# Performance work log

Hardware: AMD Instinct MI355X
Metric: run time of the kernel (lower is better)

The kernel has to match this reference:

```python
import jax, jax.numpy as jnp
import numpy as np

B, N_FED, INPUT_DIM, LATENT_DIM = 8192, 16384, 1024, 512


def setup_inputs() -> dict:
    key = jax.random.key(0)
    k1, k2, k3 = jax.random.split(key, 3)
    enc = jax.random.normal(k1, (B, LATENT_DIM), dtype=jnp.float32)
    X_fed = jax.random.normal(k2, (N_FED, INPUT_DIM), dtype=jnp.float32)
    # torch.rand -> uniform [0, 1)
    domain_diff = jax.random.uniform(k3, (INPUT_DIM, LATENT_DIM), dtype=jnp.float32)
    return {"enc": enc, "X_fed": X_fed, "domain_diff": domain_diff}


def reference(enc, X_fed, domain_diff):
    # K = V = X_fed @ domain_diff  (computed once; torch source computes it twice)
    kv = X_fed @ domain_diff                      # (N_fed, latent)
    scores = jnp.einsum('bd,nd->bn', enc, kv) / enc.shape[1]  # scale by latent_dim
    attn = jax.nn.softmax(scores, axis=1)         # softmax over N_fed axis
    z = attn @ kv                                 # (B, latent)
    return z
```

## Files before the change

kernel.cpp:

```cpp
#include <hip/hip_runtime.h>
#include <hip/hip_bf16.h>
#include <stdint.h>

#define ENC_B 8192
#define NFED  16384
#define INDIM 1024
#define LAT   512
#define SCALE (1.0f/512.0f)

typedef __attribute__((ext_vector_type(4))) float f32x4;
typedef __attribute__((ext_vector_type(8))) short short8;
typedef __attribute__((ext_vector_type(4))) short short4_t;

static __device__ __forceinline__ short f2bf(float x){
  union { float f; uint32_t u; } v; v.f = x;
  uint32_t r = v.u + 0x7FFFu + ((v.u >> 16) & 1u);
  return (short)(r >> 16);
}
static __device__ __forceinline__ float bf2f(short s){
  union { float f; uint32_t u; } v; v.u = ((uint32_t)(unsigned short)s) << 16; return v.f;
}

static __device__ __forceinline__ void gload16(const void* g, void* l){
  __builtin_amdgcn_global_load_lds(
      (const __attribute__((address_space(1))) void*)g,
      (__attribute__((address_space(3))) void*)l, 16, 0, 0);
}

__global__ void ddT_kernel(const float* __restrict__ dd, short* __restrict__ ddT){
  const int n = blockIdx.x;
  for (int k = threadIdx.x; k < INDIM; k += 256)
    ddT[(size_t)n*INDIM + k] = f2bf(dd[(size_t)k*LAT + n]);
}

__global__ __launch_bounds__(256) void encb_kernel(const float* __restrict__ enc,
                                                   short* __restrict__ encb){
  const int gid = blockIdx.x*256 + threadIdx.x;
  const size_t base = (size_t)gid * 8;
  float4 v0 = *(const float4*)(enc + base);
  float4 v1 = *(const float4*)(enc + base + 4);
  short8 s;
  s[0]=f2bf(v0.x*SCALE); s[1]=f2bf(v0.y*SCALE); s[2]=f2bf(v0.z*SCALE); s[3]=f2bf(v0.w*SCALE);
  s[4]=f2bf(v1.x*SCALE); s[5]=f2bf(v1.y*SCALE); s[6]=f2bf(v1.z*SCALE); s[7]=f2bf(v1.w*SCALE);
  *(short8*)(encb + base) = s;
}

__global__ __launch_bounds__(256, 2) void kv_gemm_kernel(const float* __restrict__ X,
                                                         const short* __restrict__ ddT,
                                                         short* __restrict__ kv){
  __shared__ __align__(16) short As[128*40];
  __shared__ __align__(16) short Bs[128*40];
  const int t = threadIdx.x;
  const int lane = t & 63, w = t >> 6;
  const int lr = lane & 15, lg = lane >> 4;
  const int m0 = (blockIdx.x >> 2) * 128;
  const int n0 = (blockIdx.x & 3) * 128;
  const int wm = (w >> 1) * 64, wn = (w & 1) * 64;
  f32x4 acc[4][4];
  #pragma unroll
  for (int i=0;i<4;++i)
    #pragma unroll
    for (int j=0;j<4;++j) acc[i][j] = (f32x4){0.f,0.f,0.f,0.f};

  for (int k0 = 0; k0 < INDIM; k0 += 32) {
    #pragma unroll
    for (int i = 0; i < 4; ++i) {
      int idx = t + i*256;
      int row = idx >> 3, c4 = (idx & 7)*4;
      float4 v = *(const float4*)(X + (size_t)(m0+row)*INDIM + k0 + c4);
      short4_t s; s[0]=f2bf(v.x); s[1]=f2bf(v.y); s[2]=f2bf(v.z); s[3]=f2bf(v.w);
      *(short4_t*)(As + row*40 + c4) = s;
    }
    #pragma unroll
    for (int i = 0; i < 2; ++i) {
      int idx = t + i*256;
      int row = idx >> 2, c8 = (idx & 3)*8;
      *(uint4*)(Bs + row*40 + c8) = *(const uint4*)(ddT + (size_t)(n0+row)*INDIM + k0 + c8);
    }
    __syncthreads();
    short8 a[4], b[4];
    #pragma unroll
    for (int i=0;i<4;++i) a[i] = *(short8*)(As + (wm + i*16 + lr)*40 + lg*8);
    #pragma unroll
    for (int i=0;i<4;++i) b[i] = *(short8*)(Bs + (wn + i*16 + lr)*40 + lg*8);
    #pragma unroll
    for (int i=0;i<4;++i)
      #pragma unroll
      for (int j=0;j<4;++j)
        acc[i][j] = __builtin_amdgcn_mfma_f32_16x16x32_bf16(a[i], b[j], acc[i][j], 0,0,0);
    __syncthreads();
  }
  #pragma unroll
  for (int i=0;i<4;++i)
    #pragma unroll
    for (int j=0;j<4;++j)
      #pragma unroll
      for (int r=0;r<4;++r)
        kv[(size_t)(m0 + wm + i*16 + lg*4 + r)*LAT + n0 + wn + j*16 + lr] = f2bf(acc[i][j][r]);
}

__global__ __launch_bounds__(256) void kvT_kernel(const short* __restrict__ kv,
                                                  short* __restrict__ kvT){
  __shared__ short tile[64][72];
  const int t = threadIdx.x;
  const int bn = blockIdx.x & (NFED/64 - 1);
  const int bd = blockIdx.x / (NFED/64);
  #pragma unroll
  for (int i=0;i<2;++i){
    int idx = t + i*256; int row = idx >> 3, cc = (idx & 7)*8;
    *(uint4*)&tile[row][cc] = *(const uint4*)(kv + (size_t)(bn*64+row)*LAT + bd*64 + cc);
  }
  __syncthreads();
  #pragma unroll
  for (int i=0;i<2;++i){
    int idx = t + i*256; int drow = idx >> 3, nn = (idx & 7)*8;
    short8 v;
    #pragma unroll
    for (int j=0;j<8;++j) v[j] = tile[nn+j][drow];
    *(short8*)(kvT + (size_t)(bd*64+drow)*NFED + bn*64 + nn) = v;
  }
}

__global__ __launch_bounds__(256, 4) void s_gemm_kernel(const short* __restrict__ encb,
                                                        const short* __restrict__ kv,
                                                        short* __restrict__ Pc,
                                                        float* __restrict__ lpart,
                                                        int cbase, int chunk){
  __shared__ __align__(16) short As[128*32];
  __shared__ __align__(16) short Bs[128*32];
  __shared__ float lsum[128][2];
  const int t = threadIdx.x;
  const int lane = t & 63, w = t >> 6;
  const int lr = lane & 15, lg = lane >> 4;
  const int m0 = blockIdx.y * 128;
  const int n0g = cbase + blockIdx.x * 128;
  const int wm = (w >> 1) * 64, wn = (w & 1) * 64;

  const int sr = lane >> 2, sc = (lane & 3) * 8;
  const char* Asrc0 = (const char*)(encb + (size_t)(m0 + w*16      + sr)*LAT + sc);
  const char* Asrc1 = (const char*)(encb + (size_t)(m0 + (4+w)*16  + sr)*LAT + sc);
  const char* Bsrc0 = (const char*)(kv   + (size_t)(n0g + w*16     + sr)*LAT + sc);
  const char* Bsrc1 = (const char*)(kv   + (size_t)(n0g + (4+w)*16 + sr)*LAT + sc);
  char* AsD0 = (char*)As + w*1024;  char* AsD1 = (char*)As + (4+w)*1024;
  char* BsD0 = (char*)Bs + w*1024;  char* BsD1 = (char*)Bs + (4+w)*1024;

  f32x4 acc[4][4];
  #pragma unroll
  for (int i=0;i<4;++i)
    #pragma unroll
    for (int j=0;j<4;++j) acc[i][j] = (f32x4){0.f,0.f,0.f,0.f};

  for (int k0 = 0; k0 < LAT; k0 += 32) {
    gload16(Asrc0, AsD0); gload16(Asrc1, AsD1);
    gload16(Bsrc0, BsD0); gload16(Bsrc1, BsD1);
    Asrc0 += 64; Asrc1 += 64; Bsrc0 += 64; Bsrc1 += 64;
    __syncthreads();
    short8 a[4], b[4];
    #pragma unroll
    for (int i=0;i<4;++i) a[i] = *(short8*)((char*)As + (wm + i*16 + lr)*64 + lg*16);
    #pragma unroll
    for (int i=0;i<4;++i) b[i] = *(short8*)((char*)Bs + (wn + i*16 + lr)*64 + lg*16);
    #pragma unroll
    for (int i=0;i<4;++i)
      #pragma unroll
      for (int j=0;j<4;++j)
        acc[i][j] = __builtin_amdgcn_mfma_f32_16x16x32_bf16(a[i], b[j], acc[i][j], 0,0,0);
    __syncthreads();
  }

  float psum[4][4];
  #pragma unroll
  for (int i=0;i<4;++i)
    #pragma unroll
    for (int r=0;r<4;++r) psum[i][r] = 0.f;

  const int collocal0 = blockIdx.x * 128 + wn;
  #pragma unroll
  for (int i=0;i<4;++i)
    #pragma unroll
    for (int j=0;j<4;++j)
      #pragma unroll
      for (int r=0;r<4;++r) {
        float p = __expf(acc[i][j][r]);
        psum[i][r] += p;
        Pc[(size_t)(m0 + wm + i*16 + lg*4 + r)*chunk + collocal0 + j*16 + lr] = f2bf(p);
      }
  #pragma unroll
  for (int i=0;i<4;++i)
    #pragma unroll
    for (int r=0;r<4;++r) {
      float v = psum[i][r];
      v += __shfl_xor(v, 1, 16); v += __shfl_xor(v, 2, 16);
      v += __shfl_xor(v, 4, 16); v += __shfl_xor(v, 8, 16);
      if (lr == 0) lsum[wm + i*16 + lg*4 + r][w & 1] = v;
    }
  __syncthreads();
  if (t < 128) {
    int jsl = (cbase >> 7) + blockIdx.x;
    lpart[(size_t)jsl*ENC_B + m0 + t] = lsum[t][0] + lsum[t][1];
  }
}

__global__ __launch_bounds__(256, 4) void z_gemm_kernel(const short* __restrict__ kvT,
                                                        const short* __restrict__ Pc,
                                                        short* __restrict__ zb,
                                                        int cbase, int chunk,
                                                        int sliceBase, int first){
  __shared__ __align__(16) short As[64*64];
  __shared__ __align__(16) short Bs[128*64];
  const int t = threadIdx.x;
  const int lane = t & 63, w = t >> 6;
  const int lr = lane & 15, lg = lane >> 4;
  const int n0 = blockIdx.x * 128;
  const int m0 = blockIdx.y * 64;
  const int s  = blockIdx.z;
  const int sl = sliceBase + s;
  const int klocal0 = s * (chunk >> 1);

  const short* Asrc[2];
  #pragma unroll
  for (int i=0;i<2;++i){
    int ca = i*256 + w*64 + lane;
    int row = ca >> 3;
    int kcs = (lane & 7) ^ (row & 7);
    Asrc[i] = kvT + (size_t)(m0 + row)*NFED + cbase + klocal0 + kcs*8;
  }
  const short* Bsrc[4];
  #pragma unroll
  for (int i=0;i<4;++i){
    int ca = i*256 + w*64 + lane;
    int row = ca >> 3;
    int kcs = (lane & 7) ^ (row & 7);
    Bsrc[i] = Pc + (size_t)(n0 + row)*chunk + klocal0 + kcs*8;
  }

  f32x4 acc[2][4];
  #pragma unroll
  for (int i=0;i<2;++i)
    #pragma unroll
    for (int j=0;j<4;++j) acc[i][j] = (f32x4){0.f,0.f,0.f,0.f};

  const int ksteps = chunk >> 7;
  for (int ks = 0; ks < ksteps; ++ks) {
    #pragma unroll
    for (int i=0;i<2;++i){
      gload16(Asrc[i], (char*)As + i*4096 + w*1024);
      Asrc[i] += 64;
    }
    #pragma unroll
    for (int i=0;i<4;++i){
      gload16(Bsrc[i], (char*)Bs + i*4096 + w*1024);
      Bsrc[i] += 64;
    }
    __syncthreads();

    #pragma unroll
    for (int kk=0;kk<2;++kk){
      const uint32_t kbyte = kk*64 + lg*16;
      short8 a[4], b[2];
      #pragma unroll
      for (int dj=0;dj<4;++dj){
        int row = dj*16 + lr;
        a[dj] = *(short8*)((char*)As + row*128 + (kbyte ^ ((uint32_t)(row & 7) << 4)));
      }
      #pragma unroll
      for (int ri=0;ri<2;++ri){
        int row = w*32 + ri*16 + lr;
        b[ri] = *(short8*)((char*)Bs + row*128 + (kbyte ^ ((uint32_t)(row & 7) << 4)));
      }
      #pragma unroll
      for (int ri=0;ri<2;++ri)
        #pragma unroll
        for (int dj=0;dj<4;++dj)
          acc[ri][dj] = __builtin_amdgcn_mfma_f32_16x16x32_bf16(a[dj], b[ri], acc[ri][dj], 0,0,0);
    }
    __syncthreads();
  }

  #pragma unroll
  for (int ri=0;ri<2;++ri)
    #pragma unroll
    for (int dj=0;dj<4;++dj)
      #pragma unroll
      for (int r=0;r<4;++r) {
        int d    = m0 + dj*16 + lg*4 + r;
        int rowq = n0 + w*32 + ri*16 + lr;
        size_t idx = ((size_t)sl*LAT + d)*ENC_B + rowq;
        float v = acc[ri][dj][r];
        if (!first) v += bf2f(zb[idx]);
        zb[idx] = f2bf(v);
      }
}

__global__ __launch_bounds__(256) void lred_kernel(const float* __restrict__ lpart,
                                                   float* __restrict__ linv){
  const int row = blockIdx.x*256 + threadIdx.x;
  float sum = 0.f;
  for (int j = 0; j < NFED/128; ++j)
    sum += lpart[(size_t)j*ENC_B + row];
  linv[row] = 1.0f / sum;
}

__global__ __launch_bounds__(256) void zcomb_kernel(const short* __restrict__ zb,
                                                    const float* __restrict__ linv,
                                                    float* __restrict__ out){
  __shared__ float tile[64][65];
  const int t = threadIdx.x;
  const int bx = blockIdx.x;
  const int by = blockIdx.y;
  #pragma unroll
  for (int i=0;i<4;++i){
    int idx = t + i*256;
    int dr = idx >> 4, rc = (idx & 15)*4;
    float s0=0.f, s1=0.f, s2=0.f, s3=0.f;
    #pragma unroll
    for (int sl=0; sl<8; ++sl){
      short4_t v = *(const short4_t*)(zb + ((size_t)sl*LAT + by*64 + dr)*ENC_B + bx*64 + rc);
      s0 += bf2f(v[0]); s1 += bf2f(v[1]); s2 += bf2f(v[2]); s3 += bf2f(v[3]);
    }
    tile[dr][rc+0]=s0; tile[dr][rc+1]=s1; tile[dr][rc+2]=s2; tile[dr][rc+3]=s3;
  }
  __syncthreads();
  #pragma unroll
  for (int i=0;i<4;++i){
    int idx = t + i*256;
    int rr = idx >> 4, dc = (idx & 15)*4;
    float li = linv[bx*64 + rr];
    float4 o;
    o.x = tile[dc+0][rr]*li; o.y = tile[dc+1][rr]*li;
    o.z = tile[dc+2][rr]*li; o.w = tile[dc+3][rr]*li;
    *(float4*)(out + (size_t)(bx*64+rr)*LAT + by*64 + dc) = o;
  }
}

extern "C" void kernel_launch(void* const* d_in, const int* in_sizes, int n_in,
                              void* d_out, int out_size, void* d_ws, size_t ws_size,
                              hipStream_t stream) {
  const float* enc = (const float*)d_in[0];
  const float* X   = (const float*)d_in[1];
  const float* dd  = (const float*)d_in[2];
  float* out = (float*)d_out;

  short* kvb   = (short*)d_ws;
  short* kvT   = (short*)((char*)d_ws + 16777216);
  short* encb  = (short*)((char*)d_ws + 33554432);
  float* lpart = (float*)((char*)d_ws + 41943040);
  short* ddT   = (short*)((char*)d_ws + 41943040);
  float* linv  = (float*)((char*)d_ws + 46137344);
  short* zb    = (short*)((char*)d_ws + 50331648);
  short* Pc    = (short*)((char*)d_ws + 117440512);

  int chunk;
  if      (ws_size >= (size_t)117440512 + (size_t)4096*ENC_B*2) chunk = 4096;
  else if (ws_size >= (size_t)117440512 + (size_t)2048*ENC_B*2) chunk = 2048;
  else                                                          chunk = 1024;

  ddT_kernel<<<LAT, 256, 0, stream>>>(dd, ddT);
  kv_gemm_kernel<<<(NFED/128)*(LAT/128), 256, 0, stream>>>(X, ddT, kvb);
  kvT_kernel<<<(NFED/64)*(LAT/64), 256, 0, stream>>>(kvb, kvT);
  encb_kernel<<<ENC_B*LAT/(256*8), 256, 0, stream>>>(enc, encb);

  const int nc = NFED / chunk;
  for (int c = 0; c < nc; ++c) {
    s_gemm_kernel<<<dim3(chunk/128, ENC_B/128), 256, 0, stream>>>(
        encb, kvb, Pc, lpart, c*chunk, chunk);
    z_gemm_kernel<<<dim3(ENC_B/128, LAT/64, 2), 256, 0, stream>>>(
        kvT, Pc, zb, c*chunk, chunk, (c & 3)*2, (c < 4) ? 1 : 0);
  }
  lred_kernel<<<ENC_B/256, 256, 0, stream>>>(lpart, linv);
  zcomb_kernel<<<dim3(ENC_B/64, LAT/64), 256, 0, stream>>>(zb, linv, out);
}
```

Before: 435.8 us.

## Enlarge score GEMM tile to 256x256 with double-buffered LDS and coalesced P stores

Result: slower. 446.2 us (+2.4%).

```diff
diff --git a/kernel.cpp b/kernel.cpp
--- a/kernel.cpp
+++ b/kernel.cpp
@@ -121,83 +121,149 @@
   }
 }
 
-__global__ __launch_bounds__(256, 4) void s_gemm_kernel(const short* __restrict__ encb,
+__global__ __launch_bounds__(512, 2) void s_gemm_kernel(const short* __restrict__ encb,
                                                         const short* __restrict__ kv,
                                                         short* __restrict__ Pc,
                                                         float* __restrict__ lpart,
                                                         int cbase, int chunk){
-  __shared__ __align__(16) short As[128*32];
-  __shared__ __align__(16) short Bs[128*32];
-  __shared__ float lsum[128][2];
+  __shared__ __align__(16) char lds[65536];
   const int t = threadIdx.x;
   const int lane = t & 63, w = t >> 6;
   const int lr = lane & 15, lg = lane >> 4;
-  const int m0 = blockIdx.y * 128;
-  const int n0g = cbase + blockIdx.x * 128;
-  const int wm = (w >> 1) * 64, wn = (w & 1) * 64;
-
-  const int sr = lane >> 2, sc = (lane & 3) * 8;
-  const char* Asrc0 = (const char*)(encb + (size_t)(m0 + w*16      + sr)*LAT + sc);
-  const char* Asrc1 = (const char*)(encb + (size_t)(m0 + (4+w)*16  + sr)*LAT + sc);
-  const char* Bsrc0 = (const char*)(kv   + (size_t)(n0g + w*16     + sr)*LAT + sc);
-  const char* Bsrc1 = (const char*)(kv   + (size_t)(n0g + (4+w)*16 + sr)*LAT + sc);
-  char* AsD0 = (char*)As + w*1024;  char* AsD1 = (char*)As + (4+w)*1024;
-  char* BsD0 = (char*)Bs + w*1024;  char* BsD1 = (char*)Bs + (4+w)*1024;
-
-  f32x4 acc[4][4];
-  #pragma unroll
-  for (int i=0;i<4;++i)
+  const int wm = w >> 2, wn = w & 3;
+  const int m0 = blockIdx.y * 256;
+  const int n0g = cbase + blockIdx.x * 256;
+
+  const short* asrc[2]; const short* bsrc[2];
+  uint32_t adst[2], bdst[2];
+  #pragma unroll
+  for (int i=0;i<2;++i){
+    int c = i*512 + w*64 + lane;
+    int row = c >> 2, kc = c & 3;
+    asrc[i] = encb + (size_t)(m0 + row)*LAT + kc*8;
+    bsrc[i] = kv   + (size_t)(n0g + row)*LAT + kc*8;
+    adst[i] = (uint32_t)((i*512 + w*64)*16);
+    bdst[i] = (uint32_t)(16384 + (i*512 + w*64)*16);
+  }
+
+  f32x4 acc[8][4];
+  #pragma unroll
+  for (int i=0;i<8;++i)
     #pragma unroll
     for (int j=0;j<4;++j) acc[i][j] = (f32x4){0.f,0.f,0.f,0.f};
 
-  for (int k0 = 0; k0 < LAT; k0 += 32) {
-    gload16(Asrc0, AsD0); gload16(Asrc1, AsD1);
-    gload16(Bsrc0, BsD0); gload16(Bsrc1, BsD1);
-    Asrc0 += 64; Asrc1 += 64; Bsrc0 += 64; Bsrc1 += 64;
-    __syncthreads();
+  #pragma unroll
+  for (int i=0;i<2;++i){ gload16(asrc[i], lds + adst[i]); gload16(bsrc[i], lds + bdst[i]); }
+  #pragma unroll
+  for (int i=0;i<2;++i){ gload16(asrc[i]+32, lds + 32768 + adst[i]);
+                         gload16(bsrc[i]+32, lds + 32768 + bdst[i]); }
+  asm volatile("s_waitcnt vmcnt(4)" ::: "memory");
+  __builtin_amdgcn_sched_barrier(0);
+  __builtin_amdgcn_s_barrier();
+  __builtin_amdgcn_sched_barrier(0);
+
+  for (int kt = 0; kt < 16; ++kt){
+    const uint32_t abase = (uint32_t)((kt & 1) << 15);
     short8 a[4], b[4];
     #pragma unroll
-    for (int i=0;i<4;++i) a[i] = *(short8*)((char*)As + (wm + i*16 + lr)*64 + lg*16);
-    #pragma unroll
-    for (int i=0;i<4;++i) b[i] = *(short8*)((char*)Bs + (wn + i*16 + lr)*64 + lg*16);
-    #pragma unroll
-    for (int i=0;i<4;++i)
-      #pragma unroll
-      for (int j=0;j<4;++j)
-        acc[i][j] = __builtin_amdgcn_mfma_f32_16x16x32_bf16(a[i], b[j], acc[i][j], 0,0,0);
-    __syncthreads();
-  }
-
-  float psum[4][4];
-  #pragma unroll
-  for (int i=0;i<4;++i)
+    for (int ni=0;ni<4;++ni)
+      b[ni] = *(short8*)(lds + abase + 16384u + (uint32_t)((wn*64 + ni*16 + lr)*64 + lg*16));
+    #pragma unroll
+    for (int mi=0;mi<4;++mi)
+      a[mi] = *(short8*)(lds + abase + (uint32_t)((wm*128 + mi*16 + lr)*64 + lg*16));
+    __builtin_amdgcn_s_setprio(1);
+    #pragma unroll
+    for (int mi=0;mi<4;++mi)
+      #pragma unroll
+      for (int ni=0;ni<4;++ni)
+        acc[mi][ni] = __builtin_amdgcn_mfma_f32_16x16x32_bf16(a[mi], b[ni], acc[mi][ni], 0,0,0);
+    __builtin_amdgcn_s_setprio(0);
+    #pragma unroll
+    for (int mi=0;mi<4;++mi)
+      a[mi] = *(short8*)(lds + abase + (uint32_t)((wm*128 + (mi+4)*16 + lr)*64 + lg*16));
+    __builtin_amdgcn_s_setprio(1);
+    #pragma unroll
+    for (int mi=0;mi<4;++mi)
+      #pragma unroll
+      for (int ni=0;ni<4;++ni)
+        acc[mi+4][ni] = __builtin_amdgcn_mfma_f32_16x16x32_bf16(a[mi], b[ni], acc[mi+4][ni], 0,0,0);
+    __builtin_amdgcn_s_setprio(0);
+
+    asm volatile("s_waitcnt lgkmcnt(0)" ::: "memory");
+    __builtin_amdgcn_sched_barrier(0);
+    __builtin_amdgcn_s_barrier();
+    __builtin_amdgcn_sched_barrier(0);
+    if (kt < 14){
+      const int ko = (kt+2)*32;
+      #pragma unroll
+      for (int i=0;i<2;++i){
+        gload16(asrc[i] + ko, lds + abase + adst[i]);
+        gload16(bsrc[i] + ko, lds + abase + bdst[i]);
+      }
+      asm volatile("s_waitcnt vmcnt(4)" ::: "memory");
+    } else {
+      asm volatile("s_waitcnt vmcnt(0)" ::: "memory");
+    }
+    __builtin_amdgcn_sched_barrier(0);
+    __builtin_amdgcn_s_barrier();
+    __builtin_amdgcn_sched_barrier(0);
+  }
+
+  float psum[8][4];
+  #pragma unroll
+  for (int i=0;i<8;++i)
     #pragma unroll
     for (int r=0;r<4;++r) psum[i][r] = 0.f;
 
-  const int collocal0 = blockIdx.x * 128 + wn;
-  #pragma unroll
-  for (int i=0;i<4;++i)
-    #pragma unroll
-    for (int j=0;j<4;++j)
-      #pragma unroll
-      for (int r=0;r<4;++r) {
-        float p = __expf(acc[i][j][r]);
-        psum[i][r] += p;
-        Pc[(size_t)(m0 + wm + i*16 + lg*4 + r)*chunk + collocal0 + j*16 + lr] = f2bf(p);
-      }
-  #pragma unroll
-  for (int i=0;i<4;++i)
-    #pragma unroll
-    for (int r=0;r<4;++r) {
-      float v = psum[i][r];
-      v += __shfl_xor(v, 1, 16); v += __shfl_xor(v, 2, 16);
-      v += __shfl_xor(v, 4, 16); v += __shfl_xor(v, 8, 16);
-      if (lr == 0) lsum[wm + i*16 + lg*4 + r][w & 1] = v;
-    }
+  #pragma unroll
+  for (int p=0;p<2;++p){
+    if (wm == p){
+      #pragma unroll
+      for (int mi=0;mi<8;++mi)
+        #pragma unroll
+        for (int ni=0;ni<4;++ni)
+          #pragma unroll
+          for (int rr=0;rr<4;++rr){
+            float pe = __expf(acc[mi][ni][rr]);
+            psum[mi][rr] += pe;
+            uint32_t row = (uint32_t)(mi*16 + lg*4 + rr);
+            uint32_t col = (uint32_t)(wn*64 + ni*16 + lr);
+            *(short*)(lds + row*512 + ((col*2) ^ (((row>>2)&3)<<5))) = f2bf(pe);
+          }
+    }
+    __syncthreads();
+    #pragma unroll
+    for (int i=0;i<8;++i){
+      uint32_t c = (uint32_t)(i*512 + t);
+      uint32_t row = c >> 5, col16 = c & 31;
+      short8 v = *(short8*)(lds + row*512 + ((col16*16) ^ (((row>>2)&3)<<5)));
+      *(short8*)(Pc + (size_t)(m0 + p*128 + row)*chunk + blockIdx.x*256 + col16*8) = v;
+    }
+    __syncthreads();
+  }
+
+  #pragma unroll
+  for (int mi=0;mi<8;++mi)
+    #pragma unroll
+    for (int rr=0;rr<4;++rr){
+      float v = psum[mi][rr];
+      v += __shfl_xor(v, 1, 64); v += __shfl_xor(v, 2, 64);
+      v += __shfl_xor(v, 4, 64); v += __shfl_xor(v, 8, 64);
+      psum[mi][rr] = v;
+    }
+  float* lsum = (float*)lds;
+  if (lr == 0){
+    #pragma unroll
+    for (int mi=0;mi<8;++mi)
+      #pragma unroll
+      for (int rr=0;rr<4;++rr)
+        lsum[(wm*128 + mi*16 + lg*4 + rr)*4 + wn] = psum[mi][rr];
+  }
   __syncthreads();
-  if (t < 128) {
-    int jsl = (cbase >> 7) + blockIdx.x;
-    lpart[(size_t)jsl*ENC_B + m0 + t] = lsum[t][0] + lsum[t][1];
+  if (t < 256){
+    float s = lsum[t*4] + lsum[t*4+1] + lsum[t*4+2] + lsum[t*4+3];
+    int jsl = (cbase >> 8) + blockIdx.x;
+    lpart[(size_t)jsl*ENC_B + m0 + t] = s;
   }
 }
 
@@ -296,7 +362,7 @@
                                                    float* __restrict__ linv){
   const int row = blockIdx.x*256 + threadIdx.x;
   float sum = 0.f;
-  for (int j = 0; j < NFED/128; ++j)
+  for (int j = 0; j < NFED/256; ++j)
     sum += lpart[(size_t)j*ENC_B + row];
   linv[row] = 1.0f / sum;
 }
@@ -362,7 +428,7 @@
 
   const int nc = NFED / chunk;
   for (int c = 0; c < nc; ++c) {
-    s_gemm_kernel<<<dim3(chunk/128, ENC_B/128), 256, 0, stream>>>(
+    s_gemm_kernel<<<dim3(chunk/256, ENC_B/256), 512, 0, stream>>>(
         encb, kvb, Pc, lpart, c*chunk, chunk);
     z_gemm_kernel<<<dim3(ENC_B/128, LAT/64, 2), 256, 0, stream>>>(
         kvT, Pc, zb, c*chunk, chunk, (c & 3)*2, (c < 4) ? 1 : 0);
```

## Restructure score GEMM with swizzled 64-wide K tiles and transposed output mapping

Applied to the files above, without the earlier changes.

New measurement: 448.1 us. +2.8%, slower.

```diff
diff --git a/kernel.cpp b/kernel.cpp
--- a/kernel.cpp
+++ b/kernel.cpp
@@ -126,78 +126,90 @@
                                                         short* __restrict__ Pc,
                                                         float* __restrict__ lpart,
                                                         int cbase, int chunk){
-  __shared__ __align__(16) short As[128*32];
-  __shared__ __align__(16) short Bs[128*32];
-  __shared__ float lsum[128][2];
+  __shared__ __align__(16) short As[128*64];
+  __shared__ __align__(16) short Bs[128*64];
+  __shared__ float lsum[128];
   const int t = threadIdx.x;
   const int lane = t & 63, w = t >> 6;
   const int lr = lane & 15, lg = lane >> 4;
-  const int m0 = blockIdx.y * 128;
   const int n0g = cbase + blockIdx.x * 128;
-  const int wm = (w >> 1) * 64, wn = (w & 1) * 64;
-
-  const int sr = lane >> 2, sc = (lane & 3) * 8;
-  const char* Asrc0 = (const char*)(encb + (size_t)(m0 + w*16      + sr)*LAT + sc);
-  const char* Asrc1 = (const char*)(encb + (size_t)(m0 + (4+w)*16  + sr)*LAT + sc);
-  const char* Bsrc0 = (const char*)(kv   + (size_t)(n0g + w*16     + sr)*LAT + sc);
-  const char* Bsrc1 = (const char*)(kv   + (size_t)(n0g + (4+w)*16 + sr)*LAT + sc);
-  char* AsD0 = (char*)As + w*1024;  char* AsD1 = (char*)As + (4+w)*1024;
-  char* BsD0 = (char*)Bs + w*1024;  char* BsD1 = (char*)Bs + (4+w)*1024;
-
-  f32x4 acc[4][4];
-  #pragma unroll
-  for (int i=0;i<4;++i)
-    #pragma unroll
-    for (int j=0;j<4;++j) acc[i][j] = (f32x4){0.f,0.f,0.f,0.f};
-
-  for (int k0 = 0; k0 < LAT; k0 += 32) {
-    gload16(Asrc0, AsD0); gload16(Asrc1, AsD1);
-    gload16(Bsrc0, BsD0); gload16(Bsrc1, BsD1);
-    Asrc0 += 64; Asrc1 += 64; Bsrc0 += 64; Bsrc1 += 64;
-    __syncthreads();
-    short8 a[4], b[4];
-    #pragma unroll
-    for (int i=0;i<4;++i) a[i] = *(short8*)((char*)As + (wm + i*16 + lr)*64 + lg*16);
-    #pragma unroll
-    for (int i=0;i<4;++i) b[i] = *(short8*)((char*)Bs + (wn + i*16 + lr)*64 + lg*16);
-    #pragma unroll
-    for (int i=0;i<4;++i)
-      #pragma unroll
-      for (int j=0;j<4;++j)
-        acc[i][j] = __builtin_amdgcn_mfma_f32_16x16x32_bf16(a[i], b[j], acc[i][j], 0,0,0);
-    __syncthreads();
-  }
-
-  float psum[4][4];
-  #pragma unroll
-  for (int i=0;i<4;++i)
-    #pragma unroll
-    for (int r=0;r<4;++r) psum[i][r] = 0.f;
-
-  const int collocal0 = blockIdx.x * 128 + wn;
-  #pragma unroll
-  for (int i=0;i<4;++i)
-    #pragma unroll
-    for (int j=0;j<4;++j)
-      #pragma unroll
-      for (int r=0;r<4;++r) {
-        float p = __expf(acc[i][j][r]);
-        psum[i][r] += p;
-        Pc[(size_t)(m0 + wm + i*16 + lg*4 + r)*chunk + collocal0 + j*16 + lr] = f2bf(p);
-      }
-  #pragma unroll
-  for (int i=0;i<4;++i)
-    #pragma unroll
-    for (int r=0;r<4;++r) {
-      float v = psum[i][r];
-      v += __shfl_xor(v, 1, 16); v += __shfl_xor(v, 2, 16);
-      v += __shfl_xor(v, 4, 16); v += __shfl_xor(v, 8, 16);
-      if (lr == 0) lsum[wm + i*16 + lg*4 + r][w & 1] = v;
-    }
+  const int m0  = blockIdx.y * 128;
+
+  const short* asrc[4]; const short* bsrc[4];
+  #pragma unroll
+  for (int i=0;i<4;++i){
+    int ca = i*256 + w*64 + lane;
+    int row = ca >> 3;
+    int kcs = (lane & 7) ^ (row & 7);
+    asrc[i] = kv   + (size_t)(n0g + row)*LAT + kcs*8;
+    bsrc[i] = encb + (size_t)(m0  + row)*LAT + kcs*8;
+  }
+
+  f32x4 acc[2][8];
+  #pragma unroll
+  for (int i=0;i<2;++i)
+    #pragma unroll
+    for (int j=0;j<8;++j) acc[i][j] = (f32x4){0.f,0.f,0.f,0.f};
+
+  for (int ks = 0; ks < 8; ++ks){
+    #pragma unroll
+    for (int i=0;i<4;++i){
+      gload16(asrc[i], (char*)As + i*4096 + w*1024);
+      gload16(bsrc[i], (char*)Bs + i*4096 + w*1024);
+      asrc[i] += 64; bsrc[i] += 64;
+    }
+    __syncthreads();
+
+    #pragma unroll
+    for (int kk=0;kk<2;++kk){
+      const uint32_t kbyte = (uint32_t)(kk*64 + lg*16);
+      short8 b[2];
+      #pragma unroll
+      for (int ri=0;ri<2;++ri){
+        int row = w*32 + ri*16 + lr;
+        b[ri] = *(short8*)((char*)Bs + row*128 + (kbyte ^ ((uint32_t)(row & 7) << 4)));
+      }
+      #pragma unroll
+      for (int h=0;h<2;++h){
+        short8 a[4];
+        #pragma unroll
+        for (int j=0;j<4;++j){
+          int row = (h*4 + j)*16 + lr;
+          a[j] = *(short8*)((char*)As + row*128 + (kbyte ^ ((uint32_t)(row & 7) << 4)));
+        }
+        #pragma unroll
+        for (int ri=0;ri<2;++ri)
+          #pragma unroll
+          for (int j=0;j<4;++j)
+            acc[ri][h*4+j] = __builtin_amdgcn_mfma_f32_16x16x32_bf16(a[j], b[ri], acc[ri][h*4+j], 0,0,0);
+      }
+    }
+    __syncthreads();
+  }
+
+  #pragma unroll
+  for (int ri=0;ri<2;++ri){
+    const int q = m0 + w*32 + ri*16 + lr;
+    float ps = 0.f;
+    #pragma unroll
+    for (int dj=0;dj<8;++dj){
+      short4_t pv;
+      #pragma unroll
+      for (int r=0;r<4;++r){
+        float pe = __expf(acc[ri][dj][r]);
+        ps += pe;
+        pv[r] = f2bf(pe);
+      }
+      *(short4_t*)(Pc + (size_t)q*chunk + blockIdx.x*128 + dj*16 + lg*4) = pv;
+    }
+    ps += __shfl_xor(ps, 16, 64);
+    ps += __shfl_xor(ps, 32, 64);
+    if (lg == 0) lsum[w*32 + ri*16 + lr] = ps;
+  }
   __syncthreads();
-  if (t < 128) {
+  if (t < 128){
     int jsl = (cbase >> 7) + blockIdx.x;
-    lpart[(size_t)jsl*ENC_B + m0 + t] = lsum[t][0] + lsum[t][1];
+    lpart[(size_t)jsl*ENC_B + m0 + t] = lsum[t];
   }
 }
 
```
